# Optimization experiments

Measured on AMD Instinct MI355X. Metric: run time of the kernel, lower is better.

The kernel has to match this reference:

```python
import jax, jax.numpy as jnp
import numpy as np
from jax import lax

BLOCKS, LAYERS = 2, 10
RES_CH, DL_CH, OUT_CH, IN_CH, K = 32, 32, 256, 1, 2
B, L = 4, 65536
W_SCALE = 0.05


def conv1d(x, w, b, dilation=1, padding=0):
    # x: [B, Cin, L], w: [Cout, Cin, K], b: [Cout]
    out = lax.conv_general_dilated(
        x, w, window_strides=(1,), padding=[(padding, padding)],
        rhs_dilation=(dilation,), dimension_numbers=('NCH', 'OIH', 'NCH'))
    return out + b[None, :, None]


def setup_inputs() -> dict:
    key = jax.random.key(0)
    ks = jax.random.split(key, 16)
    n = lambda k, shp: jax.random.normal(k, shp, dtype=jnp.float32) * W_SCALE
    inp = {
        'x': jax.random.normal(ks[0], (B, IN_CH, L), dtype=jnp.float32),
        'w_start': n(ks[1], (RES_CH, IN_CH, 1)),
        'b_start': n(ks[2], (RES_CH,)),
        # per-block, per-layer stacked params
        'filt_w': n(ks[3], (BLOCKS, LAYERS, DL_CH, RES_CH, K)),
        'filt_b': n(ks[4], (BLOCKS, LAYERS, DL_CH)),
        'gate_w': n(ks[5], (BLOCKS, LAYERS, DL_CH, RES_CH, K)),
        'gate_b': n(ks[6], (BLOCKS, LAYERS, DL_CH)),
        'res_w': n(ks[7], (BLOCKS, LAYERS, RES_CH, DL_CH, 1)),
        'res_b': n(ks[8], (BLOCKS, LAYERS, RES_CH)),
        'skip_w': n(ks[9], (BLOCKS, LAYERS, RES_CH, DL_CH, 1)),
        'skip_b': n(ks[10], (BLOCKS, LAYERS, RES_CH)),
        'w_end1': n(ks[11], (OUT_CH, RES_CH, 1)),
        'b_end1': n(ks[12], (OUT_CH,)),
        'w_end2': n(ks[13], (OUT_CH, OUT_CH, 1)),
        'b_end2': n(ks[14], (OUT_CH,)),
    }
    return inp


def reference(x, w_start, b_start, filt_w, filt_b, gate_w, gate_b,
              res_w, res_b, skip_w, skip_b, w_end1, b_end1, w_end2, b_end2):
    resid = conv1d(x, w_start, b_start)                    # [B, RES_CH, L]
    skip_total = jnp.zeros_like(resid)
    for blk in range(BLOCKS):
        r = resid
        skip = jnp.zeros_like(r)
        dilation = 1
        for i in range(LAYERS):
            pad = 1 if i == 0 else dilation * (K - 1) // 2
            f = conv1d(r, filt_w[blk, i], filt_b[blk, i], dilation, pad)
            g = conv1d(r, gate_w[blk, i], gate_b[blk, i], dilation, pad)
            if i == 0:  # source slices off the extra trailing sample
                f = f[:, :, :-1]
                g = g[:, :, :-1]
            layer_out = f * g  # NOTE: original forward applies no tanh/sigmoid
            skip = skip + conv1d(layer_out, skip_w[blk, i], skip_b[blk, i])
            r = r + conv1d(layer_out, res_w[blk, i], res_b[blk, i])
            dilation *= 2
        resid = r
        skip_total = skip_total + skip
    out = jax.nn.relu(skip_total)
    out = jax.nn.relu(conv1d(out, w_end1, b_end1))         # [B, OUT_CH, L]
    return conv1d(out, w_end2, b_end2)
```

## Files before the change

### kernel.cpp

```cpp
#include <hip/hip_runtime.h>

typedef unsigned short ushort_t;
typedef __attribute__((ext_vector_type(8))) short bf16x8;
typedef __attribute__((ext_vector_type(4))) float f32x4;

#define NTOK 262144

__device__ __forceinline__ float bf2f(ushort_t u) {
    union { unsigned u; float f; } v; v.u = ((unsigned)u) << 16; return v.f;
}
__device__ __forceinline__ ushort_t f2bf(float f) {
    union { float f; unsigned u; } v; v.f = f;
    unsigned r = 0x7fffu + ((v.u >> 16) & 1u);
    return (ushort_t)((v.u + r) >> 16);
}
__device__ __forceinline__ float ldany(const void* p, long i, int isf32) {
    return isf32 ? ((const float*)p)[i] : bf2f(((const ushort_t*)p)[i]);
}
__device__ __forceinline__ bf16x8 zero8() {
    bf16x8 z = {0,0,0,0,0,0,0,0}; return z;
}
__device__ __forceinline__ void mm3(f32x4& acc, bf16x8 ah, bf16x8 al,
                                    bf16x8 bh, bf16x8 bl) {
    acc = __builtin_amdgcn_mfma_f32_16x16x32_bf16(ah, bh, acc, 0, 0, 0);
    acc = __builtin_amdgcn_mfma_f32_16x16x32_bf16(ah, bl, acc, 0, 0, 0);
    acc = __builtin_amdgcn_mfma_f32_16x16x32_bf16(al, bh, acc, 0, 0, 0);
}
__device__ __forceinline__ void packP(f32x4 p0, f32x4 p1, bf16x8& bh, bf16x8& bl) {
    #pragma unroll
    for (int r = 0; r < 4; r++) {
        float v0 = p0[r], v1 = p1[r];
        ushort_t h0 = f2bf(v0), h1 = f2bf(v1);
        bh[r]     = (short)h0;
        bh[r + 4] = (short)h1;
        bl[r]     = (short)f2bf(v0 - bf2f(h0));
        bl[r + 4] = (short)f2bf(v1 - bf2f(h1));
    }
}

#define OFF_FB  122880
#define OFF_GB  123520
#define OFF_RB  124160
#define OFF_SB  124800
#define OFF_WST 125440
#define OFF_BST 125472
#define OFF_B1  133696
#define OFF_B2  199488
#define OFF_FLAG 199744
#define SKIP_OFF 262144
#define OFF_W2AH 8650752
#define OFF_W2AL 8683520
#define OFF_W1AH 8716288
#define OFF_W1AL 8720384
#define OFF_FGW  8724480
#define OFF_GGW  8765440
#define OFF_RWH  8806400
#define OFF_SWH  8826880

__device__ __forceinline__ char* rchunk(void* outb, int buf, int b) {
    return (char*)outb + (((long)buf * 32 + (long)b * 8) << 20);
}

__global__ void k_convert(const void* fw, const void* fb,
                          const void* gw, const void* gb,
                          const void* rw, const void* rb,
                          const void* sw, const void* sb,
                          const void* wst, const void* bst,
                          const void* w1, const void* b1,
                          const void* w2, const void* b2,
                          float* W) {
    __shared__ int sh;
    if (threadIdx.x == 0) sh = 0;
    __syncthreads();
    {
        const ushort_t* p = (const ushort_t*)fw;
        int f = 0;
        for (int j = 0; j < 16; j++) {
            ushort_t u = p[threadIdx.x * 16 + j];
            f |= (((u >> 7) & 0xFF) == 0xFF) ? 1 : 0;
        }
        if (f) atomicOr(&sh, 1);
    }
    __syncthreads();
    const int isf32 = sh;
    if (blockIdx.x == 0 && threadIdx.x == 0) W[OFF_FLAG] = (float)isf32;

    int tid = blockIdx.x * blockDim.x + threadIdx.x;
    int stride = gridDim.x * blockDim.x;

    ushort_t* fgp = (ushort_t*)(W + OFF_FGW);
    ushort_t* ggp = (ushort_t*)(W + OFF_GGW);
    ushort_t* rwp = (ushort_t*)(W + OFF_RWH);
    ushort_t* swp = (ushort_t*)(W + OFF_SWH);
    for (int idx = tid; idx < 20480; idx += stride) {
        int wl = idx >> 10;
        int coci = idx & 1023;
        #pragma unroll
        for (int tap = 0; tap < 2; tap++) {
            long base = (long)wl * 4096 + tap * 2048 + coci;
            float v = ldany(fw, (long)idx * 2 + tap, isf32);
            ushort_t h = f2bf(v);
            fgp[base] = h; fgp[base + 1024] = f2bf(v - bf2f(h));
            v = ldany(gw, (long)idx * 2 + tap, isf32);
            h = f2bf(v);
            ggp[base] = h; ggp[base + 1024] = f2bf(v - bf2f(h));
        }
        {
            int ci = coci & 31, co = coci >> 5;
            int p = ((ci >> 2) & 3) * 8 + ((ci >> 4) & 1) * 4 + (ci & 3);
            long base = (long)wl * 2048 + co * 32 + p;
            float v = ldany(rw, idx, isf32);
            ushort_t h = f2bf(v);
            rwp[base] = h; rwp[base + 1024] = f2bf(v - bf2f(h));
            v = ldany(sw, idx, isf32);
            h = f2bf(v);
            swp[base] = h; swp[base + 1024] = f2bf(v - bf2f(h));
        }
    }
    for (int idx = tid; idx < 640; idx += stride) {
        W[OFF_FB + idx] = ldany(fb, idx, isf32);
        W[OFF_GB + idx] = ldany(gb, idx, isf32);
        W[OFF_RB + idx] = ldany(rb, idx, isf32);
        W[OFF_SB + idx] = ldany(sb, idx, isf32);
    }
    for (int idx = tid; idx < 32; idx += stride) {
        W[OFF_WST + idx] = ldany(wst, idx, isf32);
        W[OFF_BST + idx] = ldany(bst, idx, isf32);
    }
    for (int idx = tid; idx < 256; idx += stride) {
        W[OFF_B1 + idx] = ldany(b1, idx, isf32);
        W[OFF_B2 + idx] = ldany(b2, idx, isf32);
    }
    {
        ushort_t* w2h = (ushort_t*)(W + OFF_W2AH);
        ushort_t* w2l = (ushort_t*)(W + OFF_W2AL);
        for (int idx = tid; idx < 65536; idx += stride) {
            float v = ldany(w2, idx, isf32);
            ushort_t h = f2bf(v);
            w2h[idx] = h;
            w2l[idx] = f2bf(v - bf2f(h));
        }
        ushort_t* w1h = (ushort_t*)(W + OFF_W1AH);
        ushort_t* w1l = (ushort_t*)(W + OFF_W1AL);
        for (int idx = tid; idx < 8192; idx += stride) {
            float v = ldany(w1, idx, isf32);
            ushort_t h = f2bf(v);
            w1h[idx] = h;
            w1l[idx] = f2bf(v - bf2f(h));
        }
    }
}

template<int NTX, int NWAVE, bool FIRST>
__global__ __launch_bounds__(NWAVE * 64, 2) void k_pair(const float* __restrict__ W,
                                                        const void* __restrict__ xin,
                                                        void* __restrict__ outb,
                                                        float* __restrict__ skp,
                                                        int bufin, int bufout,
                                                        int wlX, int t0X, int t1X, int TY) {
    constexpr int RTOK = NTX * NWAVE * 16;
    constexpr int RH = (RTOK - 256) / 2;
    constexpr int NCT = 16 / NWAVE;
    __shared__ __align__(16) char r1[RTOK * 128];
    __shared__ __align__(16) char sxs[256 * 128];
    const int tid = threadIdx.x;
    const int lane = tid & 63;
    const int wv = tid >> 6;
    const int l15 = lane & 15;
    const int l4 = lane >> 4;
    const int b = blockIdx.x >> 8;
    const int lbase = (blockIdx.x & 255) << 8;

    const char* __restrict__ rin = rchunk(outb, bufin, b);
    char* __restrict__ rout      = rchunk(outb, bufout, b);
    const int isf32 = FIRST ? ((W[OFF_FLAG] > 0.5f) ? 1 : 0) : 0;

    {
        const ushort_t* __restrict__ FG  = (const ushort_t*)(W + OFF_FGW) + (long)wlX * 4096;
        const ushort_t* __restrict__ GG  = (const ushort_t*)(W + OFF_GGW) + (long)wlX * 4096;
        const ushort_t* __restrict__ RWH = (const ushort_t*)(W + OFF_RWH) + (long)wlX * 2048;
        const ushort_t* __restrict__ SWH = (const ushort_t*)(W + OFF_SWH) + (long)wlX * 2048;
        bf16x8 afh[2][2], afl[2][2], agh[2][2], agl[2][2];
        #pragma unroll
        for (int tap = 0; tap < 2; tap++)
            #pragma unroll
            for (int mt = 0; mt < 2; mt++) {
                int row = (mt * 16 + l15) * 32 + l4 * 8;
                afh[tap][mt] = *(const bf16x8*)(FG + tap * 2048 + row);
                afl[tap][mt] = *(const bf16x8*)(FG + tap * 2048 + 1024 + row);
                agh[tap][mt] = *(const bf16x8*)(GG + tap * 2048 + row);
                agl[tap][mt] = *(const bf16x8*)(GG + tap * 2048 + 1024 + row);
            }
        bf16x8 ash[2], asl2[2], arh[2], arl[2];
        #pragma unroll
        for (int mt = 0; mt < 2; mt++) {
            int row = (mt * 16 + l15) * 32 + l4 * 8;
            ash[mt]  = *(const bf16x8*)(SWH + row);
            asl2[mt] = *(const bf16x8*)(SWH + 1024 + row);
            arh[mt]  = *(const bf16x8*)(RWH + row);
            arl[mt]  = *(const bf16x8*)(RWH + 1024 + row);
        }
        f32x4 fb2[2], gb2[2], sb4[2], rb4[2];
        #pragma unroll
        for (int mt = 0; mt < 2; mt++) {
            fb2[mt] = *(const f32x4*)(W + OFF_FB + wlX * 32 + mt * 16 + l4 * 4);
            gb2[mt] = *(const f32x4*)(W + OFF_GB + wlX * 32 + mt * 16 + l4 * 4);
            sb4[mt] = *(const f32x4*)(W + OFF_SB + wlX * 32 + mt * 16 + l4 * 4);
            rb4[mt] = *(const f32x4*)(W + OFF_RB + wlX * 32 + mt * 16 + l4 * 4);
        }
        float wstS[8], bstS[8], wstD[8], bstD[8];
        if (FIRST) {
            #pragma unroll
            for (int j = 0; j < 8; j++) {
                wstS[j] = W[OFF_WST + l4 * 8 + j];
                bstS[j] = W[OFF_BST + l4 * 8 + j];
                int c = (j >> 2) * 16 + l4 * 4 + (j & 3);
                wstD[j] = W[OFF_WST + c];
                bstD[j] = W[OFF_BST + c];
            }
        }
        const int offs2[2] = {t0X, t1X};
        for (int it = 0; it < NTX; it++) {
            const int rt = wv * NTX + it;
            const int tokl = lbase - RH + rt * 16 + l15;
            f32x4 fa[2] = {fb2[0], fb2[1]};
            f32x4 ga[2] = {gb2[0], gb2[1]};
            #pragma unroll
            for (int tap = 0; tap < 2; tap++) {
                int lt = tokl + offs2[tap];
                bf16x8 bh = zero8(), bl = zero8();
                if ((unsigned)lt < 65536u) {
                    if (FIRST) {
                        float xv = ldany(xin, ((long)b << 16) + lt, isf32);
                        #pragma unroll
                        for (int j = 0; j < 8; j++) {
                            float v = wstS[j] * xv + bstS[j];
                            ushort_t h = f2bf(v);
                            bh[j] = (short)h;
                            bl[j] = (short)f2bf(v - bf2f(h));
                        }
                    } else {
                        const char* rp = rin + (long)lt * 128 + l4 * 16;
                        bh = *(const bf16x8*)rp;
                        bl = *(const bf16x8*)(rp + 64);
                    }
                }
                #pragma unroll
                for (int mt = 0; mt < 2; mt++) {
                    mm3(fa[mt], afh[tap][mt], afl[tap][mt], bh, bl);
                    mm3(ga[mt], agh[tap][mt], agl[tap][mt], bh, bl);
                }
            }
            bf16x8 pbh, pbl;
            packP(fa[0] * ga[0], fa[1] * ga[1], pbh, pbl);
            f32x4 rdv[2] = {rb4[0], rb4[1]};
            mm3(rdv[0], arh[0], arl[0], pbh, pbl);
            mm3(rdv[1], arh[1], arl[1], pbh, pbl);
            float rx[8];
            if (FIRST) {
                if ((unsigned)tokl < 65536u) {
                    float xv = ldany(xin, ((long)b << 16) + tokl, isf32);
                    #pragma unroll
                    for (int j = 0; j < 8; j++) {
                        float v = wstD[j] * xv + bstD[j];
                        ushort_t h = f2bf(v);
                        rx[j] = bf2f(h) + bf2f(f2bf(v - bf2f(h)));
                    }
                } else {
                    #pragma unroll
                    for (int j = 0; j < 8; j++) rx[j] = 0.f;
                }
            } else {
                uint2 rxh[2] = {{0u,0u},{0u,0u}}, rxl[2] = {{0u,0u},{0u,0u}};
                if ((unsigned)tokl < 65536u) {
                    const char* rp = rin + (long)tokl * 128 + l4 * 8;
                    rxh[0] = *(const uint2*)(rp);
                    rxh[1] = *(const uint2*)(rp + 32);
                    rxl[0] = *(const uint2*)(rp + 64);
                    rxl[1] = *(const uint2*)(rp + 96);
                }
                #pragma unroll
                for (int mt = 0; mt < 2; mt++) {
                    rx[mt*4+0] = bf2f((ushort_t)(rxh[mt].x & 0xffffu)) + bf2f((ushort_t)(rxl[mt].x & 0xffffu));
                    rx[mt*4+1] = bf2f((ushort_t)(rxh[mt].x >> 16))     + bf2f((ushort_t)(rxl[mt].x >> 16));
                    rx[mt*4+2] = bf2f((ushort_t)(rxh[mt].y & 0xffffu)) + bf2f((ushort_t)(rxl[mt].y & 0xffffu));
                    rx[mt*4+3] = bf2f((ushort_t)(rxh[mt].y >> 16))     + bf2f((ushort_t)(rxl[mt].y >> 16));
                }
            }
            const int reltok = rt * 16 + l15;
            const int sw = (reltok & 7) << 4;
            #pragma unroll
            for (int mt = 0; mt < 2; mt++) {
                float v0 = rx[mt*4+0] + rdv[mt][0];
                float v1 = rx[mt*4+1] + rdv[mt][1];
                float v2 = rx[mt*4+2] + rdv[mt][2];
                float v3 = rx[mt*4+3] + rdv[mt][3];
                ushort_t h0 = f2bf(v0), h1 = f2bf(v1), h2 = f2bf(v2), h3 = f2bf(v3);
                uint2 ph, pl;
                ph.x = (unsigned)h0 | ((unsigned)h1 << 16);
                ph.y = (unsigned)h2 | ((unsigned)h3 << 16);
                pl.x = (unsigned)f2bf(v0 - bf2f(h0)) | ((unsigned)f2bf(v1 - bf2f(h1)) << 16);
                pl.y = (unsigned)f2bf(v2 - bf2f(h2)) | ((unsigned)f2bf(v3 - bf2f(h3)) << 16);
                *(uint2*)(r1 + ((reltok * 128 + mt * 32 + l4 * 8) ^ sw)) = ph;
                *(uint2*)(r1 + ((reltok * 128 + 64 + mt * 32 + l4 * 8) ^ sw)) = pl;
            }
            const int rel0 = rt * 16 - RH;
            if (rel0 >= 0 && rel0 < 256) {
                f32x4 sd0 = sb4[0], sd1 = sb4[1];
                mm3(sd0, ash[0], asl2[0], pbh, pbl);
                mm3(sd1, ash[1], asl2[1], pbh, pbl);
                const int ct = rel0 + l15;
                const int sws = (ct & 7) << 4;
                *(f32x4*)(sxs + ((ct * 128 + l4 * 16) ^ sws)) = sd0;
                *(f32x4*)(sxs + ((ct * 128 + 64 + l4 * 16) ^ sws)) = sd1;
            }
        }
    }
    __syncthreads();

    {
        const int wlY = wlX + 1;
        const ushort_t* __restrict__ FG  = (const ushort_t*)(W + OFF_FGW) + (long)wlY * 4096;
        const ushort_t* __restrict__ GG  = (const ushort_t*)(W + OFF_GGW) + (long)wlY * 4096;
        const ushort_t* __restrict__ RWH = (const ushort_t*)(W + OFF_RWH) + (long)wlY * 2048;
        const ushort_t* __restrict__ SWH = (const ushort_t*)(W + OFF_SWH) + (long)wlY * 2048;
        bf16x8 afh[2][2], afl[2][2], agh[2][2], agl[2][2];
        #pragma unroll
        for (int tap = 0; tap < 2; tap++)
            #pragma unroll
            for (int mt = 0; mt < 2; mt++) {
                int row = (mt * 16 + l15) * 32 + l4 * 8;
                afh[tap][mt] = *(const bf16x8*)(FG + tap * 2048 + row);
                afl[tap][mt] = *(const bf16x8*)(FG + tap * 2048 + 1024 + row);
                agh[tap][mt] = *(const bf16x8*)(GG + tap * 2048 + row);
                agl[tap][mt] = *(const bf16x8*)(GG + tap * 2048 + 1024 + row);
            }
        bf16x8 ash[2], asl2[2], arh[2], arl[2];
        #pragma unroll
        for (int mt = 0; mt < 2; mt++) {
            int row = (mt * 16 + l15) * 32 + l4 * 8;
            ash[mt]  = *(const bf16x8*)(SWH + row);
            asl2[mt] = *(const bf16x8*)(SWH + 1024 + row);
            arh[mt]  = *(const bf16x8*)(RWH + row);
            arl[mt]  = *(const bf16x8*)(RWH + 1024 + row);
        }
        f32x4 fb2[2], gb2[2], sb4[2], rb4[2];
        #pragma unroll
        for (int mt = 0; mt < 2; mt++) {
            fb2[mt] = *(const f32x4*)(W + OFF_FB + wlY * 32 + mt * 16 + l4 * 4);
            gb2[mt] = *(const f32x4*)(W + OFF_GB + wlY * 32 + mt * 16 + l4 * 4);
            sb4[mt] = *(const f32x4*)(W + OFF_SB + wlY * 32 + mt * 16 + l4 * 4);
            rb4[mt] = *(const f32x4*)(W + OFF_RB + wlY * 32 + mt * 16 + l4 * 4);
        }
        #pragma unroll
        for (int it = 0; it < NCT; it++) {
            const int tt = (wv * NCT + it) * 16 + l15;
            const int tokg = lbase + tt;
            f32x4 fa[2] = {fb2[0], fb2[1]};
            f32x4 ga[2] = {gb2[0], gb2[1]};
            #pragma unroll
            for (int tap = 0; tap < 2; tap++) {
                int dd = tap ? TY : -TY;
                int tg = tokg + dd;
                bf16x8 bh = zero8(), bl = zero8();
                if ((unsigned)tg < 65536u) {
                    int rel = tt + dd + RH;
                    int sw = (rel & 7) << 4;
                    bh = *(const bf16x8*)(r1 + ((rel * 128 + l4 * 16) ^ sw));
                    bl = *(const bf16x8*)(r1 + ((rel * 128 + 64 + l4 * 16) ^ sw));
                }
                #pragma unroll
                for (int mt = 0; mt < 2; mt++) {
                    mm3(fa[mt], afh[tap][mt], afl[tap][mt], bh, bl);
                    mm3(ga[mt], agh[tap][mt], agl[tap][mt], bh, bl);
                }
            }
            bf16x8 pbh, pbl;
            packP(fa[0] * ga[0], fa[1] * ga[1], pbh, pbl);
            f32x4 sd0 = sb4[0], sd1 = sb4[1];
            mm3(sd0, ash[0], asl2[0], pbh, pbl);
            mm3(sd1, ash[1], asl2[1], pbh, pbl);
            f32x4 rdv[2] = {rb4[0], rb4[1]};
            mm3(rdv[0], arh[0], arl[0], pbh, pbl);
            mm3(rdv[1], arh[1], arl[1], pbh, pbl);
            {
                const int swc = (tt & 7) << 4;
                f32x4 sx0 = *(const f32x4*)(sxs + ((tt * 128 + l4 * 16) ^ swc));
                f32x4 sx1 = *(const f32x4*)(sxs + ((tt * 128 + 64 + l4 * 16) ^ swc));
                float* sg = skp + ((long)b << 21) + (long)tokg * 32 + l4 * 4;
                if (FIRST) {
                    *(f32x4*)sg        = sd0 + sx0;
                    *(f32x4*)(sg + 16) = sd1 + sx1;
                } else {
                    *(f32x4*)sg        = *(const f32x4*)sg        + (sd0 + sx0);
                    *(f32x4*)(sg + 16) = *(const f32x4*)(sg + 16) + (sd1 + sx1);
                }
            }
            const int relc = tt + RH;
            const int swr = (relc & 7) << 4;
            #pragma unroll
            for (int mt = 0; mt < 2; mt++) {
                uint2 h  = *(const uint2*)(r1 + ((relc * 128 + mt * 32 + l4 * 8) ^ swr));
                uint2 lo = *(const uint2*)(r1 + ((relc * 128 + 64 + mt * 32 + l4 * 8) ^ swr));
                float v0 = bf2f((ushort_t)(h.x & 0xffffu)) + bf2f((ushort_t)(lo.x & 0xffffu)) + rdv[mt][0];
                float v1 = bf2f((ushort_t)(h.x >> 16))     + bf2f((ushort_t)(lo.x >> 16))     + rdv[mt][1];
                float v2 = bf2f((ushort_t)(h.y & 0xffffu)) + bf2f((ushort_t)(lo.y & 0xffffu)) + rdv[mt][2];
                float v3 = bf2f((ushort_t)(h.y >> 16))     + bf2f((ushort_t)(lo.y >> 16))     + rdv[mt][3];
                ushort_t h0 = f2bf(v0), h1 = f2bf(v1), h2 = f2bf(v2), h3 = f2bf(v3);
                uint2 ph, pl;
                ph.x = (unsigned)h0 | ((unsigned)h1 << 16);
                ph.y = (unsigned)h2 | ((unsigned)h3 << 16);
                pl.x = (unsigned)f2bf(v0 - bf2f(h0)) | ((unsigned)f2bf(v1 - bf2f(h1)) << 16);
                pl.y = (unsigned)f2bf(v2 - bf2f(h2)) | ((unsigned)f2bf(v3 - bf2f(h3)) << 16);
                char* op = rout + (long)tokg * 128 + mt * 32 + l4 * 8;
                *(uint2*)op        = ph;
                *(uint2*)(op + 64) = pl;
            }
        }
    }
}

__global__ __launch_bounds__(512, 4) void k_final(const float* __restrict__ W,
                                                  const float* __restrict__ skp,
                                                  void* __restrict__ outv) {
    __shared__ ushort_t h1s[128 * 256];
    const int tid = threadIdx.x;
    const int lane = tid & 63;
    const int wv = tid >> 6;
    const int wm = wv & 3;
    const int wn = wv >> 2;
    const int l15 = lane & 15;
    const int l4 = lane >> 4;
    const int isf32 = (W[OFF_FLAG] > 0.5f) ? 1 : 0;
    const int tokbase = blockIdx.x * 128 + wn * 64;

    const ushort_t* __restrict__ W1AH = (const ushort_t*)(W + OFF_W1AH);
    const ushort_t* __restrict__ W1AL = (const ushort_t*)(W + OFF_W1AL);
    const ushort_t* __restrict__ W2AH = (const ushort_t*)(W + OFF_W2AH);
    const ushort_t* __restrict__ W2AL = (const ushort_t*)(W + OFF_W2AL);

    bf16x8 bhi[4], blo[4];
    #pragma unroll
    for (int nt = 0; nt < 4; nt++) {
        int tok = tokbase + nt * 16 + l15;
        int bb = tok >> 16, ll = tok & 65535;
        const float* __restrict__ sk = skp + ((long)bb << 21) + (long)ll * 32 + l4 * 8;
        f32x4 u0 = *(const f32x4*)(sk);
        f32x4 u1 = *(const f32x4*)(sk + 4);
        bf16x8 h, o_;
        #pragma unroll
        for (int j = 0; j < 8; j++) {
            float v = (j < 4) ? u0[j] : u1[j - 4];
            v = v > 0.f ? v : 0.f;
            ushort_t hh = f2bf(v);
            h[j] = (short)hh;
            o_[j] = (short)f2bf(v - bf2f(hh));
        }
        bhi[nt] = h; blo[nt] = o_;
    }

    #pragma unroll
    for (int mt = 0; mt < 4; mt++) {
        int o0 = wm * 64 + mt * 16;
        const bf16x8 a_hi = *(const bf16x8*)(W1AH + (o0 + l15) * 32 + l4 * 8);
        const bf16x8 a_lo = *(const bf16x8*)(W1AL + (o0 + l15) * 32 + l4 * 8);
        f32x4 bias;
        #pragma unroll
        for (int r = 0; r < 4; r++) bias[r] = W[OFF_B1 + o0 + l4 * 4 + r];
        #pragma unroll
        for (int nt = 0; nt < 4; nt++) {
            f32x4 acc = bias;
            acc = __builtin_amdgcn_mfma_f32_16x16x32_bf16(a_hi, bhi[nt], acc, 0, 0, 0);
            acc = __builtin_amdgcn_mfma_f32_16x16x32_bf16(a_hi, blo[nt], acc, 0, 0, 0);
            acc = __builtin_amdgcn_mfma_f32_16x16x32_bf16(a_lo, bhi[nt], acc, 0, 0, 0);
            int ltk = wn * 64 + nt * 16 + l15;
            int ci0 = o0 + l4 * 4;
            float v0 = acc[0] > 0.f ? acc[0] : 0.f;
            float v1 = acc[1] > 0.f ? acc[1] : 0.f;
            float v2 = acc[2] > 0.f ? acc[2] : 0.f;
            float v3 = acc[3] > 0.f ? acc[3] : 0.f;
            uint2 pk;
            pk.x = (unsigned)f2bf(v0) | ((unsigned)f2bf(v1) << 16);
            pk.y = (unsigned)f2bf(v2) | ((unsigned)f2bf(v3) << 16);
            int byteoff = (ltk << 9) + (ci0 << 1);
            byteoff ^= (ltk & 7) << 4;
            *(uint2*)((char*)h1s + byteoff) = pk;
        }
    }
    __syncthreads();

    f32x4 acc[4][4];
    #pragma unroll
    for (int mt = 0; mt < 4; mt++) {
        int m0 = wm * 64 + mt * 16 + l4 * 4;
        #pragma unroll
        for (int r = 0; r < 4; r++) {
            float bv = W[OFF_B2 + m0 + r];
            #pragma unroll
            for (int nt = 0; nt < 4; nt++) acc[mt][nt][r] = bv;
        }
    }
    #pragma unroll 2
    for (int ks = 0; ks < 8; ks++) {
        bf16x8 bf[4];
        #pragma unroll
        for (int nt = 0; nt < 4; nt++) {
            int ltk = wn * 64 + nt * 16 + l15;
            int byteoff = (ltk << 9) + (ks << 6) + (l4 << 4);
            byteoff ^= (ltk & 7) << 4;
            bf[nt] = *(const bf16x8*)((const char*)h1s + byteoff);
        }
        #pragma unroll
        for (int mt = 0; mt < 4; mt++) {
            int o = wm * 64 + mt * 16 + l15;
            const bf16x8 a_hi = *(const bf16x8*)(W2AH + o * 256 + ks * 32 + l4 * 8);
            #pragma unroll
            for (int nt = 0; nt < 4; nt++)
                acc[mt][nt] = __builtin_amdgcn_mfma_f32_16x16x32_bf16(a_hi, bf[nt], acc[mt][nt], 0, 0, 0);
            const bf16x8 a_lo = *(const bf16x8*)(W2AL + o * 256 + ks * 32 + l4 * 8);
            #pragma unroll
            for (int nt = 0; nt < 4; nt++)
                acc[mt][nt] = __builtin_amdgcn_mfma_f32_16x16x32_bf16(a_lo, bf[nt], acc[mt][nt], 0, 0, 0);
        }
    }

    #pragma unroll
    for (int nt = 0; nt < 4; nt++) {
        int tok = tokbase + nt * 16 + l15;
        int bb = tok >> 16, ll = tok & 65535;
        #pragma unroll
        for (int mt = 0; mt < 4; mt++) {
            int m0 = wm * 64 + mt * 16 + l4 * 4;
            if (isf32) {
                float* ob = (float*)outv + ((long)bb << 24) + ((long)m0 << 16) + ll;
                #pragma unroll
                for (int r = 0; r < 4; r++) ob[(long)r << 16] = acc[mt][nt][r];
            } else {
                ushort_t* ob = (ushort_t*)outv + ((long)bb << 24) + ((long)m0 << 16) + ll;
                #pragma unroll
                for (int r = 0; r < 4; r++) ob[(long)r << 16] = f2bf(acc[mt][nt][r]);
            }
        }
    }
}

extern "C" void kernel_launch(void* const* d_in, const int* in_sizes, int n_in,
                              void* d_out, int out_size, void* d_ws, size_t ws_size,
                              hipStream_t stream) {
    const void* x    = d_in[0];
    const void* wst  = d_in[1];
    const void* bst  = d_in[2];
    const void* fw   = d_in[3];
    const void* fb   = d_in[4];
    const void* gw   = d_in[5];
    const void* gb   = d_in[6];
    const void* rw   = d_in[7];
    const void* rb   = d_in[8];
    const void* sw   = d_in[9];
    const void* sb   = d_in[10];
    const void* w1   = d_in[11];
    const void* b1   = d_in[12];
    const void* w2   = d_in[13];
    const void* b2   = d_in[14];

    float* W   = (float*)d_ws;
    float* skp = W + SKIP_OFF;

    k_convert<<<64, 256, 0, stream>>>(fw, fb, gw, gb, rw, rb, sw, sb,
                                      wst, bst, w1, b1, w2, b2, W);

    int cur = 0;
    for (int blk = 0; blk < 2; blk++) {
        int base = blk * 10;
        if (blk == 0) {
            k_pair<5, 4, true><<<1024, 256, 0, stream>>>(W, x, d_out, skp, 0, 0,
                                                         base + 0, -1, 0, 1);
            cur = 0;
        } else {
            k_pair<5, 4, false><<<1024, 256, 0, stream>>>(W, x, d_out, skp, cur, cur ^ 1,
                                                          base + 0, -1, 0, 1);
            cur ^= 1;
        }
        k_pair<5, 4, false><<<1024, 256, 0, stream>>>(W, x, d_out, skp, cur, cur ^ 1,
                                                      base + 2, -2, 2, 4);   cur ^= 1;
        k_pair<5, 4, false><<<1024, 256, 0, stream>>>(W, x, d_out, skp, cur, cur ^ 1,
                                                      base + 4, -8, 8, 16);  cur ^= 1;
        k_pair<6, 4, false><<<1024, 256, 0, stream>>>(W, x, d_out, skp, cur, cur ^ 1,
                                                      base + 6, -32, 32, 64); cur ^= 1;
        k_pair<6, 8, false><<<1024, 512, 0, stream>>>(W, x, d_out, skp, cur, cur ^ 1,
                                                      base + 8, -128, 128, 256); cur ^= 1;
    }
    k_final<<<NTOK / 128, 512, 0, stream>>>(W, skp, d_out);
}
```

Before: 1.031 ms.

## Fuse multiple WaveNet layers per kernel with halo recompute in shared memory

Replaces the two-layer k_pair kernel with a generic k_fuse that chains up to five dilated layers inside one block. The block recomputes a shrinking halo region and keeps residual activations in double-buffered shared memory, then writes to global only after the last layer. Skip contributions are accumulated in registers across the fused layers, and the skip buffer is read-modify-written once per launch instead of once per pair. This cuts the launch count from ten to six and reduces global residual and skip traffic, at the cost of redundant halo compute and larger shared-memory tiles.

```diff
diff --git a/kernel.cpp b/kernel.cpp
--- a/kernel.cpp
+++ b/kernel.cpp
@@ -151,35 +151,60 @@
     }
 }
 
-template<int NTX, int NWAVE, bool FIRST>
-__global__ __launch_bounds__(NWAVE * 64, 2) void k_pair(const float* __restrict__ W,
-                                                        const void* __restrict__ xin,
-                                                        void* __restrict__ outb,
-                                                        float* __restrict__ skp,
-                                                        int bufin, int bufout,
-                                                        int wlX, int t0X, int t1X, int TY) {
-    constexpr int RTOK = NTX * NWAVE * 16;
-    constexpr int RH = (RTOK - 256) / 2;
-    constexpr int NCT = 16 / NWAVE;
-    __shared__ __align__(16) char r1[RTOK * 128];
-    __shared__ __align__(16) char sxs[256 * 128];
-    const int tid = threadIdx.x;
+template<int NL, int RTILES, int NWAVE, bool FIRST>
+__global__ __launch_bounds__(NWAVE * 64, 2) void k_fuse(
+        const float* __restrict__ W, const void* __restrict__ xin,
+        void* __restrict__ outb, float* __restrict__ skp,
+        int bufin, int bufout, int wl0, int i0) {
+    constexpr int R  = RTILES * 16;
+    constexpr int RH = (R - 256) / 2;
+    constexpr int NB = (NL >= 3) ? 2 : 1;
+    constexpr int CB = RH / 16;
+    __shared__ __align__(16) char rbuf[NB][R * 128];
+    const int tid  = threadIdx.x;
     const int lane = tid & 63;
-    const int wv = tid >> 6;
-    const int l15 = lane & 15;
-    const int l4 = lane >> 4;
-    const int b = blockIdx.x >> 8;
+    const int wv   = tid >> 6;
+    const int l15  = lane & 15;
+    const int l4   = lane >> 4;
+    const int b     = blockIdx.x >> 8;
     const int lbase = (blockIdx.x & 255) << 8;
-
     const char* __restrict__ rin = rchunk(outb, bufin, b);
     char* __restrict__ rout      = rchunk(outb, bufout, b);
     const int isf32 = FIRST ? ((W[OFF_FLAG] > 0.5f) ? 1 : 0) : 0;
 
-    {
-        const ushort_t* __restrict__ FG  = (const ushort_t*)(W + OFF_FGW) + (long)wlX * 4096;
-        const ushort_t* __restrict__ GG  = (const ushort_t*)(W + OFF_GGW) + (long)wlX * 4096;
-        const ushort_t* __restrict__ RWH = (const ushort_t*)(W + OFF_RWH) + (long)wlX * 2048;
-        const ushort_t* __restrict__ SWH = (const ushort_t*)(W + OFF_SWH) + (long)wlX * 2048;
+    const int ct0 = CB + (((wv - CB) % NWAVE) + NWAVE) % NWAVE;
+    const int ct1 = ct0 + NWAVE;
+    f32x4 zz = {0.f, 0.f, 0.f, 0.f};
+    f32x4 skA0 = zz, skA1 = zz, skB0 = zz, skB1 = zz;
+
+    int nH[NL];
+    nH[NL - 1] = 0;
+    #pragma unroll
+    for (int k = NL - 2; k >= 0; k--)
+        nH[k] = nH[k + 1] + (1 << (i0 + k));
+
+    float wstS[8], bstS[8], wstD[8], bstD[8];
+    if (FIRST) {
+        #pragma unroll
+        for (int j = 0; j < 8; j++) {
+            wstS[j] = W[OFF_WST + l4 * 8 + j];
+            bstS[j] = W[OFF_BST + l4 * 8 + j];
+            int c = (j >> 2) * 16 + l4 * 4 + (j & 3);
+            wstD[j] = W[OFF_WST + c];
+            bstD[j] = W[OFF_BST + c];
+        }
+    }
+
+    #pragma unroll
+    for (int k = 0; k < NL; k++) {
+        const int wl  = wl0 + k;
+        const int i   = i0 + k;
+        const int tpb = (i == 0) ? 0 : (1 << (i - 1));
+        const int tpa = (i == 0) ? -1 : -(1 << (i - 1));
+        const ushort_t* __restrict__ FG  = (const ushort_t*)(W + OFF_FGW) + (long)wl * 4096;
+        const ushort_t* __restrict__ GG  = (const ushort_t*)(W + OFF_GGW) + (long)wl * 4096;
+        const ushort_t* __restrict__ RWH = (const ushort_t*)(W + OFF_RWH) + (long)wl * 2048;
+        const ushort_t* __restrict__ SWH = (const ushort_t*)(W + OFF_SWH) + (long)wl * 2048;
         bf16x8 afh[2][2], afl[2][2], agh[2][2], agl[2][2];
         #pragma unroll
         for (int tap = 0; tap < 2; tap++)
@@ -191,58 +216,58 @@
                 agh[tap][mt] = *(const bf16x8*)(GG + tap * 2048 + row);
                 agl[tap][mt] = *(const bf16x8*)(GG + tap * 2048 + 1024 + row);
             }
-        bf16x8 ash[2], asl2[2], arh[2], arl[2];
+        bf16x8 arh[2], arl[2];
         #pragma unroll
         for (int mt = 0; mt < 2; mt++) {
             int row = (mt * 16 + l15) * 32 + l4 * 8;
-            ash[mt]  = *(const bf16x8*)(SWH + row);
-            asl2[mt] = *(const bf16x8*)(SWH + 1024 + row);
-            arh[mt]  = *(const bf16x8*)(RWH + row);
-            arl[mt]  = *(const bf16x8*)(RWH + 1024 + row);
-        }
-        f32x4 fb2[2], gb2[2], sb4[2], rb4[2];
+            arh[mt] = *(const bf16x8*)(RWH + row);
+            arl[mt] = *(const bf16x8*)(RWH + 1024 + row);
+        }
+        f32x4 fb2[2], gb2[2], rb4[2];
         #pragma unroll
         for (int mt = 0; mt < 2; mt++) {
-            fb2[mt] = *(const f32x4*)(W + OFF_FB + wlX * 32 + mt * 16 + l4 * 4);
-            gb2[mt] = *(const f32x4*)(W + OFF_GB + wlX * 32 + mt * 16 + l4 * 4);
-            sb4[mt] = *(const f32x4*)(W + OFF_SB + wlX * 32 + mt * 16 + l4 * 4);
-            rb4[mt] = *(const f32x4*)(W + OFF_RB + wlX * 32 + mt * 16 + l4 * 4);
-        }
-        float wstS[8], bstS[8], wstD[8], bstD[8];
-        if (FIRST) {
-            #pragma unroll
-            for (int j = 0; j < 8; j++) {
-                wstS[j] = W[OFF_WST + l4 * 8 + j];
-                bstS[j] = W[OFF_BST + l4 * 8 + j];
-                int c = (j >> 2) * 16 + l4 * 4 + (j & 3);
-                wstD[j] = W[OFF_WST + c];
-                bstD[j] = W[OFF_BST + c];
-            }
-        }
-        const int offs2[2] = {t0X, t1X};
-        for (int it = 0; it < NTX; it++) {
-            const int rt = wv * NTX + it;
-            const int tokl = lbase - RH + rt * 16 + l15;
+            fb2[mt] = *(const f32x4*)(W + OFF_FB + wl * 32 + mt * 16 + l4 * 4);
+            gb2[mt] = *(const f32x4*)(W + OFF_GB + wl * 32 + mt * 16 + l4 * 4);
+            rb4[mt] = *(const f32x4*)(W + OFF_RB + wl * 32 + mt * 16 + l4 * 4);
+        }
+        const int lo_t = (RH - nH[k]) >> 4;
+        const int hi_t = (R - RH + nH[k] + 15) >> 4;
+        const char* __restrict__ inb = rbuf[(k + 1) & (NB - 1)];
+        char* __restrict__ outl = rbuf[k & (NB - 1)];
+
+        for (int t = wv; t < RTILES; t += NWAVE) {
+            if (t < lo_t || t >= hi_t) continue;
+            const int rel  = t * 16 + l15;
+            const int gtok = lbase - RH + rel;
             f32x4 fa[2] = {fb2[0], fb2[1]};
             f32x4 ga[2] = {gb2[0], gb2[1]};
             #pragma unroll
             for (int tap = 0; tap < 2; tap++) {
-                int lt = tokl + offs2[tap];
+                const int tp = tap ? tpb : tpa;
+                const int g2 = gtok + tp;
                 bf16x8 bh = zero8(), bl = zero8();
-                if ((unsigned)lt < 65536u) {
-                    if (FIRST) {
-                        float xv = ldany(xin, ((long)b << 16) + lt, isf32);
-                        #pragma unroll
-                        for (int j = 0; j < 8; j++) {
-                            float v = wstS[j] * xv + bstS[j];
-                            ushort_t h = f2bf(v);
-                            bh[j] = (short)h;
-                            bl[j] = (short)f2bf(v - bf2f(h));
+                if ((unsigned)g2 < 65536u) {
+                    if (k == 0) {
+                        if (FIRST) {
+                            float xv = ldany(xin, ((long)b << 16) + g2, isf32);
+                            #pragma unroll
+                            for (int j = 0; j < 8; j++) {
+                                float v = wstS[j] * xv + bstS[j];
+                                ushort_t h = f2bf(v);
+                                bh[j] = (short)h;
+                                bl[j] = (short)f2bf(v - bf2f(h));
+                            }
+                        } else {
+                            const char* rp = rin + (long)g2 * 128 + l4 * 16;
+                            bh = *(const bf16x8*)rp;
+                            bl = *(const bf16x8*)(rp + 64);
                         }
                     } else {
-                        const char* rp = rin + (long)lt * 128 + l4 * 16;
-                        bh = *(const bf16x8*)rp;
-                        bl = *(const bf16x8*)(rp + 64);
+                        int cr = rel + tp;
+                        cr = cr < 0 ? 0 : (cr >= R ? R - 1 : cr);
+                        const int sw2 = (cr & 7) << 4;
+                        bh = *(const bf16x8*)(inb + ((cr * 128 + l4 * 16) ^ sw2));
+                        bl = *(const bf16x8*)(inb + ((cr * 128 + 64 + l4 * 16) ^ sw2));
                     }
                 }
                 #pragma unroll
@@ -256,166 +281,109 @@
             f32x4 rdv[2] = {rb4[0], rb4[1]};
             mm3(rdv[0], arh[0], arl[0], pbh, pbl);
             mm3(rdv[1], arh[1], arl[1], pbh, pbl);
+            if (t == ct0 || t == ct1) {
+                bf16x8 ash[2], asl2[2];
+                f32x4 sb4[2];
+                #pragma unroll
+                for (int mt = 0; mt < 2; mt++) {
+                    int row = (mt * 16 + l15) * 32 + l4 * 8;
+                    ash[mt]  = *(const bf16x8*)(SWH + row);
+                    asl2[mt] = *(const bf16x8*)(SWH + 1024 + row);
+                    sb4[mt]  = *(const f32x4*)(W + OFF_SB + wl * 32 + mt * 16 + l4 * 4);
+                }
+                f32x4 sd0 = sb4[0], sd1 = sb4[1];
+                mm3(sd0, ash[0], asl2[0], pbh, pbl);
+                mm3(sd1, ash[1], asl2[1], pbh, pbl);
+                if (t == ct0) { skA0 += sd0; skA1 += sd1; }
+                else          { skB0 += sd0; skB1 += sd1; }
+            }
             float rx[8];
-            if (FIRST) {
-                if ((unsigned)tokl < 65536u) {
-                    float xv = ldany(xin, ((long)b << 16) + tokl, isf32);
-                    #pragma unroll
-                    for (int j = 0; j < 8; j++) {
-                        float v = wstD[j] * xv + bstD[j];
-                        ushort_t h = f2bf(v);
-                        rx[j] = bf2f(h) + bf2f(f2bf(v - bf2f(h)));
+            const bool gv = ((unsigned)gtok < 65536u);
+            if (k == 0) {
+                if (FIRST) {
+                    if (gv) {
+                        float xv = ldany(xin, ((long)b << 16) + gtok, isf32);
+                        #pragma unroll
+                        for (int j = 0; j < 8; j++) {
+                            float v = wstD[j] * xv + bstD[j];
+                            ushort_t h = f2bf(v);
+                            rx[j] = bf2f(h) + bf2f(f2bf(v - bf2f(h)));
+                        }
+                    } else {
+                        #pragma unroll
+                        for (int j = 0; j < 8; j++) rx[j] = 0.f;
                     }
                 } else {
+                    uint2 rxh[2] = {{0u,0u},{0u,0u}}, rxl[2] = {{0u,0u},{0u,0u}};
+                    if (gv) {
+                        const char* rp = rin + (long)gtok * 128 + l4 * 8;
+                        rxh[0] = *(const uint2*)(rp);
+                        rxh[1] = *(const uint2*)(rp + 32);
+                        rxl[0] = *(const uint2*)(rp + 64);
+                        rxl[1] = *(const uint2*)(rp + 96);
+                    }
                     #pragma unroll
-                    for (int j = 0; j < 8; j++) rx[j] = 0.f;
+                    for (int mt = 0; mt < 2; mt++) {
+                        rx[mt*4+0] = bf2f((ushort_t)(rxh[mt].x & 0xffffu)) + bf2f((ushort_t)(rxl[mt].x & 0xffffu));
+                        rx[mt*4+1] = bf2f((ushort_t)(rxh[mt].x >> 16))     + bf2f((ushort_t)(rxl[mt].x >> 16));
+                        rx[mt*4+2] = bf2f((ushort_t)(rxh[mt].y & 0xffffu)) + bf2f((ushort_t)(rxl[mt].y & 0xffffu));
+                        rx[mt*4+3] = bf2f((ushort_t)(rxh[mt].y >> 16))     + bf2f((ushort_t)(rxl[mt].y >> 16));
+                    }
                 }
             } else {
-                uint2 rxh[2] = {{0u,0u},{0u,0u}}, rxl[2] = {{0u,0u},{0u,0u}};
-                if ((unsigned)tokl < 65536u) {
-                    const char* rp = rin + (long)tokl * 128 + l4 * 8;
-                    rxh[0] = *(const uint2*)(rp);
-                    rxh[1] = *(const uint2*)(rp + 32);
-                    rxl[0] = *(const uint2*)(rp + 64);
-                    rxl[1] = *(const uint2*)(rp + 96);
-                }
+                const int sw = (rel & 7) << 4;
                 #pragma unroll
                 for (int mt = 0; mt < 2; mt++) {
-                    rx[mt*4+0] = bf2f((ushort_t)(rxh[mt].x & 0xffffu)) + bf2f((ushort_t)(rxl[mt].x & 0xffffu));
-                    rx[mt*4+1] = bf2f((ushort_t)(rxh[mt].x >> 16))     + bf2f((ushort_t)(rxl[mt].x >> 16));
-                    rx[mt*4+2] = bf2f((ushort_t)(rxh[mt].y & 0xffffu)) + bf2f((ushort_t)(rxl[mt].y & 0xffffu));
-                    rx[mt*4+3] = bf2f((ushort_t)(rxh[mt].y >> 16))     + bf2f((ushort_t)(rxl[mt].y >> 16));
+                    uint2 h2 = {0u,0u}, lo2 = {0u,0u};
+                    if (gv) {
+                        h2  = *(const uint2*)(inb + ((rel * 128 + mt * 32 + l4 * 8) ^ sw));
+                        lo2 = *(const uint2*)(inb + ((rel * 128 + 64 + mt * 32 + l4 * 8) ^ sw));
+                    }
+                    rx[mt*4+0] = bf2f((ushort_t)(h2.x & 0xffffu)) + bf2f((ushort_t)(lo2.x & 0xffffu));
+                    rx[mt*4+1] = bf2f((ushort_t)(h2.x >> 16))     + bf2f((ushort_t)(lo2.x >> 16));
+                    rx[mt*4+2] = bf2f((ushort_t)(h2.y & 0xffffu)) + bf2f((ushort_t)(lo2.y & 0xffffu));
+                    rx[mt*4+3] = bf2f((ushort_t)(h2.y >> 16))     + bf2f((ushort_t)(lo2.y >> 16));
                 }
             }
-            const int reltok = rt * 16 + l15;
-            const int sw = (reltok & 7) << 4;
             #pragma unroll
             for (int mt = 0; mt < 2; mt++) {
                 float v0 = rx[mt*4+0] + rdv[mt][0];
                 float v1 = rx[mt*4+1] + rdv[mt][1];
                 float v2 = rx[mt*4+2] + rdv[mt][2];
                 float v3 = rx[mt*4+3] + rdv[mt][3];
-                ushort_t h0 = f2bf(v0), h1 = f2bf(v1), h2 = f2bf(v2), h3 = f2bf(v3);
+                ushort_t h0 = f2bf(v0), h1 = f2bf(v1), h2_ = f2bf(v2), h3 = f2bf(v3);
                 uint2 ph, pl;
-                ph.x = (unsigned)h0 | ((unsigned)h1 << 16);
-                ph.y = (unsigned)h2 | ((unsigned)h3 << 16);
-                pl.x = (unsigned)f2bf(v0 - bf2f(h0)) | ((unsigned)f2bf(v1 - bf2f(h1)) << 16);
-                pl.y = (unsigned)f2bf(v2 - bf2f(h2)) | ((unsigned)f2bf(v3 - bf2f(h3)) << 16);
-                *(uint2*)(r1 + ((reltok * 128 + mt * 32 + l4 * 8) ^ sw)) = ph;
-                *(uint2*)(r1 + ((reltok * 128 + 64 + mt * 32 + l4 * 8) ^ sw)) = pl;
-            }
-            const int rel0 = rt * 16 - RH;
-            if (rel0 >= 0 && rel0 < 256) {
-                f32x4 sd0 = sb4[0], sd1 = sb4[1];
-                mm3(sd0, ash[0], asl2[0], pbh, pbl);
-                mm3(sd1, ash[1], asl2[1], pbh, pbl);
-                const int ct = rel0 + l15;
-                const int sws = (ct & 7) << 4;
-                *(f32x4*)(sxs + ((ct * 128 + l4 * 16) ^ sws)) = sd0;
-                *(f32x4*)(sxs + ((ct * 128 + 64 + l4 * 16) ^ sws)) = sd1;
-            }
-        }
-    }
-    __syncthreads();
-
-    {
-        const int wlY = wlX + 1;
-        const ushort_t* __restrict__ FG  = (const ushort_t*)(W + OFF_FGW) + (long)wlY * 4096;
-        const ushort_t* __restrict__ GG  = (const ushort_t*)(W + OFF_GGW) + (long)wlY * 4096;
-        const ushort_t* __restrict__ RWH = (const ushort_t*)(W + OFF_RWH) + (long)wlY * 2048;
-        const ushort_t* __restrict__ SWH = (const ushort_t*)(W + OFF_SWH) + (long)wlY * 2048;
-        bf16x8 afh[2][2], afl[2][2], agh[2][2], agl[2][2];
-        #pragma unroll
-        for (int tap = 0; tap < 2; tap++)
-            #pragma unroll
-            for (int mt = 0; mt < 2; mt++) {
-                int row = (mt * 16 + l15) * 32 + l4 * 8;
-                afh[tap][mt] = *(const bf16x8*)(FG + tap * 2048 + row);
-                afl[tap][mt] = *(const bf16x8*)(FG + tap * 2048 + 1024 + row);
-                agh[tap][mt] = *(const bf16x8*)(GG + tap * 2048 + row);
-                agl[tap][mt] = *(const bf16x8*)(GG + tap * 2048 + 1024 + row);
-            }
-        bf16x8 ash[2], asl2[2], arh[2], arl[2];
-        #pragma unroll
-        for (int mt = 0; mt < 2; mt++) {
-            int row = (mt * 16 + l15) * 32 + l4 * 8;
-            ash[mt]  = *(const bf16x8*)(SWH + row);
-            asl2[mt] = *(const bf16x8*)(SWH + 1024 + row);
-            arh[mt]  = *(const bf16x8*)(RWH + row);
-            arl[mt]  = *(const bf16x8*)(RWH + 1024 + row);
-        }
-        f32x4 fb2[2], gb2[2], sb4[2], rb4[2];
-        #pragma unroll
-        for (int mt = 0; mt < 2; mt++) {
-            fb2[mt] = *(const f32x4*)(W + OFF_FB + wlY * 32 + mt * 16 + l4 * 4);
-            gb2[mt] = *(const f32x4*)(W + OFF_GB + wlY * 32 + mt * 16 + l4 * 4);
-            sb4[mt] = *(const f32x4*)(W + OFF_SB + wlY * 32 + mt * 16 + l4 * 4);
-            rb4[mt] = *(const f32x4*)(W + OFF_RB + wlY * 32 + mt * 16 + l4 * 4);
-        }
-        #pragma unroll
-        for (int it = 0; it < NCT; it++) {
-            const int tt = (wv * NCT + it) * 16 + l15;
-            const int tokg = lbase + tt;
-            f32x4 fa[2] = {fb2[0], fb2[1]};
-            f32x4 ga[2] = {gb2[0], gb2[1]};
-            #pragma unroll
-            for (int tap = 0; tap < 2; tap++) {
-                int dd = tap ? TY : -TY;
-                int tg = tokg + dd;
-                bf16x8 bh = zero8(), bl = zero8();
-                if ((unsigned)tg < 65536u) {
-                    int rel = tt + dd + RH;
-                    int sw = (rel & 7) << 4;
-                    bh = *(const bf16x8*)(r1 + ((rel * 128 + l4 * 16) ^ sw));
-                    bl = *(const bf16x8*)(r1 + ((rel * 128 + 64 + l4 * 16) ^ sw));
-                }
-                #pragma unroll
-                for (int mt = 0; mt < 2; mt++) {
-                    mm3(fa[mt], afh[tap][mt], afl[tap][mt], bh, bl);
-                    mm3(ga[mt], agh[tap][mt], agl[tap][mt], bh, bl);
+                ph.x = (unsigned)h0  | ((unsigned)h1 << 16);
+                ph.y = (unsigned)h2_ | ((unsigned)h3 << 16);
+                pl.x = (unsigned)f2bf(v0 - bf2f(h0))  | ((unsigned)f2bf(v1 - bf2f(h1)) << 16);
+                pl.y = (unsigned)f2bf(v2 - bf2f(h2_)) | ((unsigned)f2bf(v3 - bf2f(h3)) << 16);
+                if (k < NL - 1) {
+                    const int sw = (rel & 7) << 4;
+                    *(uint2*)(outl + ((rel * 128 + mt * 32 + l4 * 8) ^ sw)) = ph;
+                    *(uint2*)(outl + ((rel * 128 + 64 + mt * 32 + l4 * 8) ^ sw)) = pl;
+                } else {
+                    char* op = rout + (long)gtok * 128 + mt * 32 + l4 * 8;
+                    *(uint2*)op        = ph;
+                    *(uint2*)(op + 64) = pl;
                 }
             }
-            bf16x8 pbh, pbl;
-            packP(fa[0] * ga[0], fa[1] * ga[1], pbh, pbl);
-            f32x4 sd0 = sb4[0], sd1 = sb4[1];
-            mm3(sd0, ash[0], asl2[0], pbh, pbl);
-            mm3(sd1, ash[1], asl2[1], pbh, pbl);
-            f32x4 rdv[2] = {rb4[0], rb4[1]};
-            mm3(rdv[0], arh[0], arl[0], pbh, pbl);
-            mm3(rdv[1], arh[1], arl[1], pbh, pbl);
-            {
-                const int swc = (tt & 7) << 4;
-                f32x4 sx0 = *(const f32x4*)(sxs + ((tt * 128 + l4 * 16) ^ swc));
-                f32x4 sx1 = *(const f32x4*)(sxs + ((tt * 128 + 64 + l4 * 16) ^ swc));
-                float* sg = skp + ((long)b << 21) + (long)tokg * 32 + l4 * 4;
-                if (FIRST) {
-                    *(f32x4*)sg        = sd0 + sx0;
-                    *(f32x4*)(sg + 16) = sd1 + sx1;
-                } else {
-                    *(f32x4*)sg        = *(const f32x4*)sg        + (sd0 + sx0);
-                    *(f32x4*)(sg + 16) = *(const f32x4*)(sg + 16) + (sd1 + sx1);
-                }
-            }
-            const int relc = tt + RH;
-            const int swr = (relc & 7) << 4;
-            #pragma unroll
-            for (int mt = 0; mt < 2; mt++) {
-                uint2 h  = *(const uint2*)(r1 + ((relc * 128 + mt * 32 + l4 * 8) ^ swr));
-                uint2 lo = *(const uint2*)(r1 + ((relc * 128 + 64 + mt * 32 + l4 * 8) ^ swr));
-                float v0 = bf2f((ushort_t)(h.x & 0xffffu)) + bf2f((ushort_t)(lo.x & 0xffffu)) + rdv[mt][0];
-                float v1 = bf2f((ushort_t)(h.x >> 16))     + bf2f((ushort_t)(lo.x >> 16))     + rdv[mt][1];
-                float v2 = bf2f((ushort_t)(h.y & 0xffffu)) + bf2f((ushort_t)(lo.y & 0xffffu)) + rdv[mt][2];
-                float v3 = bf2f((ushort_t)(h.y >> 16))     + bf2f((ushort_t)(lo.y >> 16))     + rdv[mt][3];
-                ushort_t h0 = f2bf(v0), h1 = f2bf(v1), h2 = f2bf(v2), h3 = f2bf(v3);
-                uint2 ph, pl;
-                ph.x = (unsigned)h0 | ((unsigned)h1 << 16);
-                ph.y = (unsigned)h2 | ((unsigned)h3 << 16);
-                pl.x = (unsigned)f2bf(v0 - bf2f(h0)) | ((unsigned)f2bf(v1 - bf2f(h1)) << 16);
-                pl.y = (unsigned)f2bf(v2 - bf2f(h2)) | ((unsigned)f2bf(v3 - bf2f(h3)) << 16);
-                char* op = rout + (long)tokg * 128 + mt * 32 + l4 * 8;
-                *(uint2*)op        = ph;
-                *(uint2*)(op + 64) = pl;
-            }
+        }
+        __syncthreads();
+    }
+
+    {
+        long gt0 = (long)(lbase - RH + ct0 * 16 + l15);
+        long gt1 = (long)(lbase - RH + ct1 * 16 + l15);
+        float* sg0 = skp + ((long)b << 21) + gt0 * 32 + l4 * 4;
+        float* sg1 = skp + ((long)b << 21) + gt1 * 32 + l4 * 4;
+        if (FIRST) {
+            *(f32x4*)sg0 = skA0;        *(f32x4*)(sg0 + 16) = skA1;
+            *(f32x4*)sg1 = skB0;        *(f32x4*)(sg1 + 16) = skB1;
+        } else {
+            *(f32x4*)sg0        = *(const f32x4*)sg0        + skA0;
+            *(f32x4*)(sg0 + 16) = *(const f32x4*)(sg0 + 16) + skA1;
+            *(f32x4*)sg1        = *(const f32x4*)sg1        + skB0;
+            *(f32x4*)(sg1 + 16) = *(const f32x4*)(sg1 + 16) + skB1;
         }
     }
 }
@@ -569,26 +537,12 @@
     k_convert<<<64, 256, 0, stream>>>(fw, fb, gw, gb, rw, rb, sw, sb,
                                       wst, bst, w1, b1, w2, b2, W);
 
-    int cur = 0;
-    for (int blk = 0; blk < 2; blk++) {
-        int base = blk * 10;
-        if (blk == 0) {
-            k_pair<5, 4, true><<<1024, 256, 0, stream>>>(W, x, d_out, skp, 0, 0,
-                                                         base + 0, -1, 0, 1);
-            cur = 0;
-        } else {
-            k_pair<5, 4, false><<<1024, 256, 0, stream>>>(W, x, d_out, skp, cur, cur ^ 1,
-                                                          base + 0, -1, 0, 1);
-            cur ^= 1;
-        }
-        k_pair<5, 4, false><<<1024, 256, 0, stream>>>(W, x, d_out, skp, cur, cur ^ 1,
-                                                      base + 2, -2, 2, 4);   cur ^= 1;
-        k_pair<5, 4, false><<<1024, 256, 0, stream>>>(W, x, d_out, skp, cur, cur ^ 1,
-                                                      base + 4, -8, 8, 16);  cur ^= 1;
-        k_pair<6, 4, false><<<1024, 256, 0, stream>>>(W, x, d_out, skp, cur, cur ^ 1,
-                                                      base + 6, -32, 32, 64); cur ^= 1;
-        k_pair<6, 8, false><<<1024, 512, 0, stream>>>(W, x, d_out, skp, cur, cur ^ 1,
-                                                      base + 8, -128, 128, 256); cur ^= 1;
-    }
+    k_fuse<5, 20, 8, true ><<<1024, 512, 0, stream>>>(W, x, d_out, skp, 0, 0,  0, 0);
+    k_fuse<3, 28, 8, false><<<1024, 512, 0, stream>>>(W, x, d_out, skp, 0, 1,  5, 5);
+    k_fuse<2, 48, 8, false><<<1024, 512, 0, stream>>>(W, x, d_out, skp, 1, 0,  8, 8);
+    k_fuse<5, 20, 8, false><<<1024, 512, 0, stream>>>(W, x, d_out, skp, 0, 1, 10, 0);
+    k_fuse<3, 28, 8, false><<<1024, 512, 0, stream>>>(W, x, d_out, skp, 1, 0, 15, 5);
+    k_fuse<2, 48, 8, false><<<1024, 512, 0, stream>>>(W, x, d_out, skp, 0, 1, 18, 8);
+
     k_final<<<NTOK / 128, 512, 0, stream>>>(W, skp, d_out);
 }
```

Measured after the change: 1.091 ms. +5.8%, slower.
